# Performance work log

Measured on AMD Instinct MI355X. Metric: run time of the kernel, lower is better.

## Reference

```python
import jax, jax.numpy as jnp
import numpy as np

_THR = 0.008856  # OpenCV Lab threshold (6/29)^3


def _f_lab(t):
    # f(t) = t^(1/3) if t > thr else 7.787*t + 16/116 ; safe-where avoids nan/inf grads at 0
    safe = jnp.where(t > _THR, t, 1.0)
    return jnp.where(t > _THR, jnp.cbrt(safe), 7.787 * t + 16.0 / 116.0)


def _rgb_to_lab(img):
    """img: [B,3,H,W] in [0,1] -> OpenCV 8-bit-scaled Lab, divided by 255 (as in the torch code)."""
    img = jnp.clip(img, 0.0, 1.0)  # blur mixes channels so values can exceed 1; cv2 path saturates to 8-bit range
    r, g, b = img[:, 0], img[:, 1], img[:, 2]
    # linear RGB -> XYZ (OpenCV matrix), with white-point normalization of X and Z
    X = (0.412453 * r + 0.357580 * g + 0.180423 * b) / 0.950456
    Y = 0.212671 * r + 0.715160 * g + 0.072169 * b
    Z = (0.019334 * r + 0.119193 * g + 0.950227 * b) / 1.088754
    fX, fY, fZ = _f_lab(X), _f_lab(Y), _f_lab(Z)
    safeY = jnp.where(Y > _THR, Y, 1.0)
    L = jnp.where(Y > _THR, 116.0 * jnp.cbrt(safeY) - 16.0, 903.3 * Y)
    a = 500.0 * (fX - fY) + 128.0
    bb = 200.0 * (fY - fZ) + 128.0
    # OpenCV 8-bit scaling: L*255/100, a+128, b+128 ; torch code then divides by 255
    lab = jnp.stack([L * 255.0 / 100.0, a, bb], axis=1) / 255.0
    return lab


def _blur(img, weight):
    # F.conv2d with ones(3,3,5,5)/25, padding=2: each output channel is the SUM over input
    # channels of the 5x5 mean (full channel mixing, as in the torch module).
    return jax.lax.conv_general_dilated(
        img, weight, window_strides=(1, 1), padding=[(2, 2), (2, 2)],
        dimension_numbers=("NCHW", "OIHW", "NCHW"))


def setup_inputs() -> dict:
    key = jax.random.key(0)
    k1, k2 = jax.random.split(key)
    B, C, H, W = 32, 3, 512, 512
    img1 = jax.random.uniform(k1, (B, C, H, W), dtype=jnp.float32)
    img2 = jax.random.uniform(k2, (B, C, H, W), dtype=jnp.float32)
    kernel_size = 5
    weight = jnp.ones((3, 3, kernel_size, kernel_size), dtype=jnp.float32) / (kernel_size ** 2)
    return {"img1": img1, "img2": img2, "weight": weight}


def reference(img1, img2, weight):
    lab1 = _rgb_to_lab(_blur(img1, weight))
    lab2 = _rgb_to_lab(_blur(img2, weight))
    return jnp.mean((lab1 - lab2) ** 2)  # F.mse_loss, reduction='mean'
```

## Files before the change

### kernel.cpp

```cpp
#include <hip/hip_runtime.h>


constexpr int TILE  = 64;
constexpr int HALO  = 2;
constexpr int EXT   = TILE + 2 * HALO;
constexpr int IMG_H = 512;
constexpr int IMG_W = 512;
constexpr int BATCH = 32;
constexpr float THR = 0.008856f;

__global__ __launch_bounds__(256)
void lcol_mse_kernel(const float* __restrict__ img1,
                     const float* __restrict__ img2,
                     const float* __restrict__ weight,
                     float* __restrict__ out)
{
    __shared__ float cs[EXT * EXT];
    __shared__ float hb[2][EXT * TILE];
    __shared__ float wpart[4];

    const int tid = threadIdx.x;
    const int bx0 = blockIdx.x * TILE;
    const int by0 = blockIdx.y * TILE;
    const int b   = blockIdx.z;

    const float w0 = weight[0];

    const size_t plane = (size_t)IMG_H * IMG_W;
    const float* bases[2] = { img1 + (size_t)b * 3 * plane,
                              img2 + (size_t)b * 3 * plane };

    for (int img = 0; img < 2; ++img) {
        const float* base = bases[img];
        for (int i = tid; i < EXT * EXT; i += 256) {
            int row = i / EXT;
            int col = i - row * EXT;
            int gy = by0 + row - HALO;
            int gx = bx0 + col - HALO;
            float v = 0.f;
            if ((unsigned)gy < (unsigned)IMG_H && (unsigned)gx < (unsigned)IMG_W) {
                size_t o = (size_t)gy * IMG_W + gx;
                v = base[o] + base[plane + o] + base[2 * plane + o];
            }
            cs[i] = v;
        }
        __syncthreads();
        float* h = hb[img];
        for (int i = tid; i < EXT * TILE; i += 256) {
            int y = i >> 6;
            int x = i & 63;
            const float* r = &cs[y * EXT + x];
            h[i] = r[0] + r[1] + r[2] + r[3] + r[4];
        }
        __syncthreads();
    }

    float acc = 0.f;
    #pragma unroll
    for (int k = 0; k < 16; ++k) {
        int i = tid + k * 256;
        int y = i >> 6;
        int x = i & 63;
        const float* p1 = &hb[0][y * TILE + x];
        const float* p2 = &hb[1][y * TILE + x];
        float v1 = (p1[0] + p1[TILE] + p1[2*TILE] + p1[3*TILE] + p1[4*TILE]) * w0;
        float v2 = (p2[0] + p2[TILE] + p2[2*TILE] + p2[3*TILE] + p2[4*TILE]) * w0;
        v1 = fminf(fmaxf(v1, 0.f), 1.f);
        v2 = fminf(fmaxf(v2, 0.f), 1.f);
        float L1 = (v1 > THR) ? (116.f * cbrtf(v1) - 16.f) : (903.3f * v1);
        float L2 = (v2 > THR) ? (116.f * cbrtf(v2) - 16.f) : (903.3f * v2);
        float d = L1 - L2;
        acc += d * d;
    }

    #pragma unroll
    for (int off = 32; off; off >>= 1) acc += __shfl_down(acc, off);
    if ((tid & 63) == 0) wpart[tid >> 6] = acc;
    __syncthreads();
    if (tid == 0) {
        float s = wpart[0] + wpart[1] + wpart[2] + wpart[3];
        const float scale = (float)(1.0 / (10000.0 * (double)BATCH * 3.0 * IMG_H * IMG_W));
        atomicAdd(out, s * scale);
    }
}

extern "C" void kernel_launch(void* const* d_in, const int* in_sizes, int n_in,
                              void* d_out, int out_size, void* d_ws, size_t ws_size,
                              hipStream_t stream) {
    const float* img1   = (const float*)d_in[0];
    const float* img2   = (const float*)d_in[1];
    const float* weight = (const float*)d_in[2];
    float* out = (float*)d_out;

    hipMemsetAsync(out, 0, sizeof(float), stream);

    dim3 grid(IMG_W / TILE, IMG_H / TILE, BATCH);
    lcol_mse_kernel<<<grid, dim3(256), 0, stream>>>(img1, img2, weight, out);
}
```

Baseline: 262.9 us.

## Vectorize tile loads and use register sliding-window vertical blur

Global loads of the channel-summed halo tile now use float4 over a padded 72-column shared buffer instead of scalar loads. The horizontal-pass shared buffers are removed: each thread computes horizontal sums on the fly and keeps a rolling window of five row sums in registers while walking 16 rows vertically. Image-1 L values are held in a per-thread register array until image 2 is processed. The aim is fewer memory instructions, less shared memory and higher occupancy (launch bounds now request 8 blocks), at the cost of more registers per thread.

```diff
diff --git a/kernel.cpp b/kernel.cpp
--- a/kernel.cpp
+++ b/kernel.cpp
@@ -3,74 +3,77 @@
 
 constexpr int TILE  = 64;
 constexpr int HALO  = 2;
-constexpr int EXT   = TILE + 2 * HALO;
+constexpr int ROWS  = TILE + 2 * HALO;
+constexpr int CPAD  = 72;
+constexpr int NF4   = CPAD / 4;
 constexpr int IMG_H = 512;
 constexpr int IMG_W = 512;
 constexpr int BATCH = 32;
 constexpr float THR = 0.008856f;
 
-__global__ __launch_bounds__(256)
+__global__ __launch_bounds__(256, 8)
 void lcol_mse_kernel(const float* __restrict__ img1,
                      const float* __restrict__ img2,
                      const float* __restrict__ weight,
                      float* __restrict__ out)
 {
-    __shared__ float cs[EXT * EXT];
-    __shared__ float hb[2][EXT * TILE];
+    __shared__ float cs[ROWS * CPAD];
     __shared__ float wpart[4];
 
     const int tid = threadIdx.x;
     const int bx0 = blockIdx.x * TILE;
     const int by0 = blockIdx.y * TILE;
     const int b   = blockIdx.z;
-
-    const float w0 = weight[0];
+    const float wtap = weight[0];
 
     const size_t plane = (size_t)IMG_H * IMG_W;
     const float* bases[2] = { img1 + (size_t)b * 3 * plane,
                               img2 + (size_t)b * 3 * plane };
 
+    const int x  = tid & 63;
+    const int r0 = (tid >> 6) * 16;
+
+    float L1[16];
+    float acc = 0.f;
+
     for (int img = 0; img < 2; ++img) {
         const float* base = bases[img];
-        for (int i = tid; i < EXT * EXT; i += 256) {
-            int row = i / EXT;
-            int col = i - row * EXT;
-            int gy = by0 + row - HALO;
-            int gx = bx0 + col - HALO;
-            float v = 0.f;
+
+        for (int n = tid; n < ROWS * NF4; n += 256) {
+            int row = n / NF4;
+            int k   = n - row * NF4;
+            int gy  = by0 + row - HALO;
+            int gx  = bx0 + 4 * k - 4;
+            float4 v = make_float4(0.f, 0.f, 0.f, 0.f);
             if ((unsigned)gy < (unsigned)IMG_H && (unsigned)gx < (unsigned)IMG_W) {
-                size_t o = (size_t)gy * IMG_W + gx;
-                v = base[o] + base[plane + o] + base[2 * plane + o];
+                const float* p = base + (size_t)gy * IMG_W + gx;
+                float4 r  = *(const float4*)(p);
+                float4 g  = *(const float4*)(p + plane);
+                float4 bl = *(const float4*)(p + 2 * plane);
+                v = make_float4(r.x + g.x + bl.x, r.y + g.y + bl.y,
+                                r.z + g.z + bl.z, r.w + g.w + bl.w);
             }
-            cs[i] = v;
+            *(float4*)&cs[row * CPAD + 4 * k] = v;
         }
         __syncthreads();
-        float* h = hb[img];
-        for (int i = tid; i < EXT * TILE; i += 256) {
-            int y = i >> 6;
-            int x = i & 63;
-            const float* r = &cs[y * EXT + x];
-            h[i] = r[0] + r[1] + r[2] + r[3] + r[4];
+
+        const float* colbase = &cs[x + 2];
+        float h0 = colbase[(r0    ) * CPAD] + colbase[(r0    ) * CPAD + 1] + colbase[(r0    ) * CPAD + 2] + colbase[(r0    ) * CPAD + 3] + colbase[(r0    ) * CPAD + 4];
+        float h1 = colbase[(r0 + 1) * CPAD] + colbase[(r0 + 1) * CPAD + 1] + colbase[(r0 + 1) * CPAD + 2] + colbase[(r0 + 1) * CPAD + 3] + colbase[(r0 + 1) * CPAD + 4];
+        float h2 = colbase[(r0 + 2) * CPAD] + colbase[(r0 + 2) * CPAD + 1] + colbase[(r0 + 2) * CPAD + 2] + colbase[(r0 + 2) * CPAD + 3] + colbase[(r0 + 2) * CPAD + 4];
+        float h3 = colbase[(r0 + 3) * CPAD] + colbase[(r0 + 3) * CPAD + 1] + colbase[(r0 + 3) * CPAD + 2] + colbase[(r0 + 3) * CPAD + 3] + colbase[(r0 + 3) * CPAD + 4];
+        #pragma unroll
+        for (int k = 0; k < 16; ++k) {
+            const float* p = colbase + (r0 + 4 + k) * CPAD;
+            float h4 = p[0] + p[1] + p[2] + p[3] + p[4];
+            float v  = (h0 + h1 + h2 + h3 + h4) * wtap;
+            v = fminf(fmaxf(v, 0.f), 1.f);
+            float L = (v > THR) ? (116.f * cbrtf(v) - 16.f) : (903.3f * v);
+            if (img == 0) L1[k] = L;
+            else { float d = L1[k] - L; acc += d * d; }
+            h0 = h1; h1 = h2; h2 = h3; h3 = h4;
         }
         __syncthreads();
-    }
-
-    float acc = 0.f;
-    #pragma unroll
-    for (int k = 0; k < 16; ++k) {
-        int i = tid + k * 256;
-        int y = i >> 6;
-        int x = i & 63;
-        const float* p1 = &hb[0][y * TILE + x];
-        const float* p2 = &hb[1][y * TILE + x];
-        float v1 = (p1[0] + p1[TILE] + p1[2*TILE] + p1[3*TILE] + p1[4*TILE]) * w0;
-        float v2 = (p2[0] + p2[TILE] + p2[2*TILE] + p2[3*TILE] + p2[4*TILE]) * w0;
-        v1 = fminf(fmaxf(v1, 0.f), 1.f);
-        v2 = fminf(fmaxf(v2, 0.f), 1.f);
-        float L1 = (v1 > THR) ? (116.f * cbrtf(v1) - 16.f) : (903.3f * v1);
-        float L2 = (v2 > THR) ? (116.f * cbrtf(v2) - 16.f) : (903.3f * v2);
-        float d = L1 - L2;
-        acc += d * d;
     }
 
     #pragma unroll
```

After: 235.0 us. -10.6%, faster.
